# Performance work log

Hardware: AMD Instinct MI355X
Metric: run time of the kernel (lower is better)

## Reference

```python
import jax, jax.numpy as jnp
import numpy as np

S, N, LAT, HID, NH, NLAYERS = 8, 128, 128, 384, 8, 6
HT, WT, DT = 128, 128, 128
DIN, DOUT, RAD, LEVELS, FED = 1169, 3 + 3 * 128, 3, 4, 64


def sincos1d(d, pos):
    # MAE-style 1d sincos embedding, d even -> [..., d]
    omega = 1.0 / (10000.0 ** (jnp.arange(d // 2, dtype=jnp.float32) / (d / 2.0)))
    ang = pos[..., None] * omega
    return jnp.concatenate([jnp.sin(ang), jnp.cos(ang)], axis=-1)


def flow_embed(f, Cd=FED):
    # get_3d_embedding(flows, 64, cat_coords=True) -> [..., 3*Cd+3] = 195
    div = jnp.arange(0, Cd, 2, dtype=jnp.float32) * (1000.0 / Cd)
    outs = []
    for a in range(3):
        ang = f[..., a, None] * div
        pe = jnp.stack([jnp.sin(ang), jnp.cos(ang)], axis=-1).reshape(f.shape[:-1] + (Cd,))
        outs.append(pe)
    return jnp.concatenate(outs + [f], axis=-1)


def avg_pool2(x):
    B, Sv, Cc, H, W = x.shape
    return x.reshape(B, Sv, Cc, H // 2, 2, W // 2, 2).mean(axis=(4, 6))


def pyramid(fm):
    pyr = [fm]
    for _ in range(LEVELS - 1):
        fm = avg_pool2(fm)
        pyr.append(fm)
    return pyr


def bilinear_sample(corr, xy):
    # corr: [B,S,N,H,W]; xy: [B,S,N,P,2] pixel coords (x indexes W, y indexes H); zero padding
    B, Sv, Nn, H, W = corr.shape
    cf = corr.reshape(B, Sv, Nn, H * W)
    x, y = xy[..., 0], xy[..., 1]
    x0f = jnp.floor(x); y0f = jnp.floor(y)
    wx, wy = x - x0f, y - y0f
    x0 = x0f.astype(jnp.int32); y0 = y0f.astype(jnp.int32)

    def gather(xi, yi):
        ok = ((xi >= 0) & (xi < W) & (yi >= 0) & (yi < H)).astype(cf.dtype)
        idx = jnp.clip(yi, 0, H - 1) * W + jnp.clip(xi, 0, W - 1)
        v = jnp.take_along_axis(cf, idx.reshape(B, Sv, Nn, -1), axis=-1).reshape(idx.shape)
        return v * ok

    v00 = gather(x0, y0); v01 = gather(x0 + 1, y0)
    v10 = gather(x0, y0 + 1); v11 = gather(x0 + 1, y0 + 1)
    return v00 * (1 - wx) * (1 - wy) + v01 * wx * (1 - wy) + v10 * (1 - wx) * wy + v11 * wx * wy


def corr_sample(pyr, targets, coords):
    # RAFT/CoTracker CorrBlock: per-level dense correlation then (2r+1)^2 window bilinear lookup
    d = jnp.arange(-RAD, RAD + 1, dtype=jnp.float32)
    delta = jnp.stack(jnp.meshgrid(d, d, indexing="ij"), axis=-1).reshape(-1, 2)  # [49,2]
    scale = 1.0 / jnp.sqrt(jnp.float32(targets.shape[-1]))
    outs = []
    for l, fm in enumerate(pyr):
        corr = jnp.einsum("bsnc,bschw->bsnhw", targets, fm) * scale
        xy = coords[..., None, :] / (2.0 ** l) + delta
        outs.append(bilinear_sample(corr, xy))
    return jnp.concatenate(outs, axis=-1)  # [B,S,N,196]


def layernorm(x, g, b):
    m = x.mean(-1, keepdims=True)
    v = x.var(-1, keepdims=True)
    return (x - m) / jnp.sqrt(v + 1e-5) * g + b


def attention(x, Wqkv, bq, Wo, bo):
    M, T, H = x.shape
    dh = H // NH
    qkv = (x @ Wqkv + bq).reshape(M, T, 3, NH, dh)
    q, k, v = qkv[:, :, 0], qkv[:, :, 1], qkv[:, :, 2]
    att = jax.nn.softmax(jnp.einsum("mthd,mshd->mhts", q, k) / jnp.sqrt(jnp.float32(dh)), axis=-1)
    o = jnp.einsum("mhts,mshd->mthd", att, v).reshape(M, T, H)
    return o @ Wo + bo


def updateformer(x, support, W_in, b_in, lnp, Wqkv, bqkv, Wo, bo, W1, b1, W2, b2, W_out, b_out, Ws, bs):
    # x: [B,N,T,DIN]; alternating time (over T) and space (over N) pre-LN transformer blocks
    B, Np, T, _ = x.shape
    sproj = support @ Ws + bs  # [100,HID]
    h = x @ W_in + b_in + sproj.mean(axis=0)
    for i in range(NLAYERS):
        g1, bb1, g2, bb2 = lnp[i, 0], lnp[i, 1], lnp[i, 2], lnp[i, 3]
        if i % 2 == 0:
            y = h.reshape(B * Np, T, HID)
        else:
            y = h.transpose(0, 2, 1, 3).reshape(B * T, Np, HID)
        y = y + attention(layernorm(y, g1, bb1), Wqkv[i], bqkv[i], Wo[i], bo[i])
        z = layernorm(y, g2, bb2)
        y = y + jax.nn.gelu(z @ W1[i] + b1[i], approximate=False) @ W2[i] + b2[i]
        if i % 2 == 0:
            h = y.reshape(B, Np, T, HID)
        else:
            h = y.reshape(B, T, Np, HID).transpose(0, 2, 1, 3)
    return h @ W_out + b_out, sproj[None]


def groupnorm1(x, g, b):
    m = x.mean(-1, keepdims=True)
    v = x.var(-1, keepdims=True)
    return (x - m) / jnp.sqrt(v + 1e-5) * g + b


def _forward(fmapXY, fmapYZ, fmapXZ, coords_init, vis_init, track_mask, feat_init, support_features,
             W_in, b_in, lnp, Wqkv, bqkv, Wo, bo, W1, b1, W2, b2, W_out, b_out, Ws, bs,
             gn_g, gn_b, Wu, bu, Wvis, bvis, iters):
    B, Sv, Cc, H, W = fmapXY.shape
    D = fmapXZ.shape[-2]
    Nn = coords_init.shape[2]
    coords = coords_init
    ffeats = [feat_init[..., k] for k in range(3)]
    pyrXY, pyrYZ, pyrXZ = pyramid(fmapXY), pyramid(fmapYZ), pyramid(fmapXZ)
    grid_size = jnp.array([H, W, D], dtype=jnp.float32)
    # 3d sincos pos embed from query coords; 1169 padded to 1170 -> 390/axis, truncated back
    g = (coords[:, 0] / grid_size * 2.0 - 1.0) * 128.0  # [B,N,3]
    pe = jnp.concatenate([sincos1d(390, g[..., i]) for i in range(3)], axis=-1)[..., :DIN]
    pos_embed = pe.reshape(B * Nn, 1, DIN)
    times_embed = sincos1d(1170, jnp.arange(Sv, dtype=jnp.float32))[None, :, :DIN]
    support = support_features
    for _ in range(iters):
        coords = jax.lax.stop_gradient(coords)  # matches coords.detach()
        fxy = corr_sample(pyrXY, ffeats[0], coords[..., :2])
        fyz = corr_sample(pyrYZ, ffeats[1], coords[..., 1:3])
        fxz = corr_sample(pyrXZ, ffeats[2], coords[..., 0::2])
        fcorrs = jnp.concatenate([fxy, fyz, fxz], axis=-1)  # [B,S,N,588]
        fcorrs_ = fcorrs.transpose(0, 2, 1, 3).reshape(B * Nn, Sv, -1)
        flows_ = (coords - coords[:, :1]).transpose(0, 2, 1, 3).reshape(B * Nn, Sv, 3)
        flows_cat = flow_embed(flows_)  # [BN,S,195]
        ff = [f.transpose(0, 2, 1, 3).reshape(B * Nn, Sv, LAT) for f in ffeats]
        ffeats_ = jnp.concatenate(ff, axis=-1)  # [BN,S,384]
        # replicate torch's cat(dim=2)+permute+reshape layout exactly
        tmv = jnp.concatenate([track_mask, vis_init], axis=2).transpose(0, 2, 1, 3).reshape(B * Nn, Sv, 2)
        tin = jnp.concatenate([flows_cat, fcorrs_, ffeats_, tmv], axis=-1)  # [BN,S,1169]
        x = (tin + pos_embed + times_embed).reshape(B, Nn, Sv, DIN)
        delta, dse3 = updateformer(x, support, W_in, b_in, lnp, Wqkv, bqkv, Wo, bo, W1, b1, W2, b2, W_out, b_out, Ws, bs)
        support = support + dse3[0] / 100.0
        delta = delta.reshape(B * Nn, Sv, DOUT)
        d_coord = delta[..., :3].reshape(B, Nn, Sv, 3).transpose(0, 2, 1, 3)
        coords = coords + d_coord
        new_ffeats = []
        for k in range(3):
            dfk = delta[..., 3 + k * LAT:3 + (k + 1) * LAT]
            upd = jax.nn.gelu(groupnorm1(dfk, gn_g[k], gn_b[k]) @ Wu[k] + bu[k], approximate=False)
            new_ffeats.append(ffeats[k] + upd.reshape(B, Nn, Sv, LAT).transpose(0, 2, 1, 3))
        ffeats = new_ffeats
    vis = (jnp.concatenate(ffeats, axis=-1) @ Wvis + bvis)[..., 0]  # [B,S,N]
    return jnp.concatenate([coords, vis[..., None]], axis=-1)  # [B,S,N,4]


def setup_inputs() -> dict:
    key = jax.random.key(0)
    ks = jax.random.split(key, 16)
    f32 = jnp.float32
    B = 1
    fmapXY = jax.random.normal(ks[0], (B, S, LAT, HT, WT), f32)
    fmapYZ = jax.random.normal(ks[1], (B, S, LAT, DT, HT), f32)
    fmapXZ = jax.random.normal(ks[2], (B, S, LAT, DT, WT), f32)
    coords_init = jax.random.uniform(ks[3], (B, S, N, 3), f32) * 112.0 + 8.0
    vis_init = jnp.ones((B, S, N, 1), f32)
    track_mask = jnp.ones((B, S, N, 1), f32)
    feat_init = jax.random.normal(ks[4], (B, S, N, LAT, 3), f32)
    support_features = jnp.zeros((100, HID), f32) + 0.1
    w = lambda k, sh: jax.random.normal(k, sh, f32) * 0.02
    ln1 = jnp.stack([jnp.ones(HID, f32), jnp.zeros(HID, f32), jnp.ones(HID, f32), jnp.zeros(HID, f32)])
    params = dict(
        W_in=w(ks[5], (DIN, HID)), b_in=jnp.zeros((HID,), f32),
        lnp=jnp.tile(ln1[None], (NLAYERS, 1, 1)),
        Wqkv=w(ks[6], (NLAYERS, HID, 3 * HID)), bqkv=jnp.zeros((NLAYERS, 3 * HID), f32),
        Wo=w(ks[7], (NLAYERS, HID, HID)), bo=jnp.zeros((NLAYERS, HID), f32),
        W1=w(ks[8], (NLAYERS, HID, 4 * HID)), b1=jnp.zeros((NLAYERS, 4 * HID), f32),
        W2=w(ks[9], (NLAYERS, 4 * HID, HID)), b2=jnp.zeros((NLAYERS, HID), f32),
        W_out=w(ks[10], (HID, DOUT)), b_out=jnp.zeros((DOUT,), f32),
        Ws=w(ks[11], (HID, HID)), bs=jnp.zeros((HID,), f32),
        gn_g=jnp.ones((3, LAT), f32), gn_b=jnp.zeros((3, LAT), f32),
        Wu=w(ks[12], (3, LAT, LAT)), bu=jnp.zeros((3, LAT), f32),
        Wvis=w(ks[13], (3 * LAT, 1)), bvis=jnp.zeros((1,), f32),
    )
    return dict(fmapXY=fmapXY, fmapYZ=fmapYZ, fmapXZ=fmapXZ, coords_init=coords_init,
                vis_init=vis_init, track_mask=track_mask, feat_init=feat_init,
                support_features=support_features, iters=2, **params)


def reference(fmapXY, fmapYZ, fmapXZ, coords_init, vis_init, track_mask, feat_init, support_features,
              W_in, b_in, lnp, Wqkv, bqkv, Wo, bo, W1, b1, W2, b2, W_out, b_out, Ws, bs,
              gn_g, gn_b, Wu, bu, Wvis, bvis, iters):
    return _forward(fmapXY, fmapYZ, fmapXZ, coords_init, vis_init, track_mask, feat_init, support_features,
                    W_in, b_in, lnp, Wqkv, bqkv, Wo, bo, W1, b1, W2, b2, W_out, b_out, Ws, bs,
                    gn_g, gn_b, Wu, bu, Wvis, bvis, iters)
```

## Files before the change

kernel.cpp:

```cpp
#include <hip/hip_runtime.h>
#include <hip/hip_bf16.h>


#define DEVFN __device__ __forceinline__

typedef __attribute__((ext_vector_type(8))) short short8;
typedef __attribute__((ext_vector_type(4))) float f32x4;

static constexpr float INV_SQRT_DH = 0.14433756729740643f;
static constexpr float CORR_SCALE  = 0.08838834764831845f;
static constexpr size_t VSTRIDE = 22282240;

DEVFN float gelu_exact(float x){
  return 0.5f * x * (1.0f + erff(x * 0.7071067811865476f));
}
DEVFN short bf16_of(float f){
  __hip_bfloat16 b = __float2bfloat16(f);
  return *reinterpret_cast<short*>(&b);
}


__global__ void init_state_k(float* coords, const float* cinit,
                             float* ff, const float* feat_init,
                             float* support, const float* sfeat){
  int idx = blockIdx.x*256 + threadIdx.x;
  if (idx < 3072)  coords[idx]  = cinit[idx];
  if (idx < 49152){
    int row = idx / 384;
    support[idx] = (row < 100) ? sfeat[idx] : 0.0f;
  }
  if (idx < 393216){
    int k = idx / 131072, rest = idx % 131072;
    ff[idx] = feat_init[(size_t)rest*3 + k];
  }
}

__global__ void build_posE_k(float* posE, const float* cinit){
  int idx = blockIdx.x*256 + threadIdx.x;
  if (idx >= 128*1169) return;
  int n = idx / 1169, d = idx % 1169;
  int i = d / 390, dd = d % 390;
  float c = cinit[n*3 + i];
  float g = (c / 128.0f * 2.0f - 1.0f) * 128.0f;
  int m = (dd < 195) ? dd : dd - 195;
  float om = powf(10000.0f, -(float)m / 195.0f);
  float ang = g * om;
  posE[idx] = (dd < 195) ? sinf(ang) : cosf(ang);
}

__global__ void build_timE_k(float* timE){
  int idx = blockIdx.x*256 + threadIdx.x;
  if (idx >= 8*1169) return;
  int s = idx / 1169, d = idx % 1169;
  int m = (d < 585) ? d : d - 585;
  float om = powf(10000.0f, -(float)m / 585.0f);
  float ang = (float)s * om;
  timE[idx] = (d < 585) ? sinf(ang) : cosf(ang);
}

__global__ void transpose_cl_k(const float* __restrict__ in, __hip_bfloat16* __restrict__ out){
  __shared__ float tile[32][33];
  int s = blockIdx.z;
  int c0 = blockIdx.y*32, h0 = blockIdx.x*32;
  int tx = threadIdx.x & 31, ty = threadIdx.x >> 5;
  const float* ib = in + (size_t)s*128*16384;
  #pragma unroll
  for (int r=0;r<4;r++){
    int c = c0 + ty + r*8;
    tile[ty + r*8][tx] = ib[(size_t)c*16384 + h0 + tx];
  }
  __syncthreads();
  __hip_bfloat16* ob = out + (size_t)s*16384*128;
  #pragma unroll
  for (int r=0;r<4;r++){
    int hw = h0 + ty + r*8;
    ob[(size_t)hw*128 + c0 + tx] = __float2bfloat16(tile[tx][ty + r*8]);
  }
}

__global__ void pool2_k(const __hip_bfloat16* __restrict__ in, __hip_bfloat16* __restrict__ out, int So){
  int idx = blockIdx.x*256 + threadIdx.x;
  int total = 8*So*So*128;
  if (idx >= total) return;
  int c = idx & 127;
  int x = (idx >> 7) % So;
  int y = ((idx >> 7) / So) % So;
  int s = idx / (So*So*128);
  int Si = So*2;
  const __hip_bfloat16* b0 = in + (((size_t)s*Si + 2*y)*Si + 2*x)*128 + c;
  float v = __bfloat162float(b0[0]) + __bfloat162float(b0[128])
          + __bfloat162float(b0[(size_t)Si*128]) + __bfloat162float(b0[(size_t)Si*128 + 128]);
  out[idx] = __float2bfloat16(v*0.25f);
}

__global__ void wtrans_k(const float* __restrict__ in, __hip_bfloat16* __restrict__ out,
                         int K, int N, int Kpad, int Npad){
  __shared__ float tile[32][33];
  int z = blockIdx.z;
  const float* ib = in + (size_t)z*K*N;
  __hip_bfloat16* ob = out + (size_t)z*Npad*Kpad;
  int kb = blockIdx.y*32, nb = blockIdx.x*32;
  int tx = threadIdx.x & 31, ty = threadIdx.x >> 5;
  #pragma unroll
  for (int r=0;r<4;r++){
    int k = kb + ty + r*8, n = nb + tx;
    tile[ty+r*8][tx] = (k < K && n < N) ? ib[(size_t)k*N + n] : 0.0f;
  }
  __syncthreads();
  #pragma unroll
  for (int r=0;r<4;r++){
    int n = nb + ty + r*8, k = kb + tx;
    if (n < Npad && k < Kpad) ob[(size_t)n*Kpad + k] = __float2bfloat16(tile[tx][ty+r*8]);
  }
}

__global__ void corr_k(const __hip_bfloat16* __restrict__ pyr, const float* __restrict__ coords,
                       const float* __restrict__ ff, float* __restrict__ xbuf){
  __shared__ float t[128];
  __shared__ float p[64];
  int bid = blockIdx.x;
  int view = bid >> 10, s = (bid >> 7) & 7, n = bid & 127;
  int tid = threadIdx.x;
  t[tid]      = ff[(size_t)view*131072 + (size_t)(s*128+n)*128 + tid];
  t[tid + 64] = ff[(size_t)view*131072 + (size_t)(s*128+n)*128 + tid + 64];
  int ax = (view==1) ? 1 : 0;
  int ay = (view==0) ? 1 : 2;
  float X = coords[(s*128+n)*3 + ax];
  float Y = coords[(s*128+n)*3 + ay];
  const __hip_bfloat16* vb = pyr + (size_t)view*VSTRIDE;
  __syncthreads();
  size_t loff = 0;
  for (int l=0;l<4;l++){
    int sz = 128 >> l;
    float inv = 1.0f / (float)(1 << l);
    float cx = X * inv, cy = Y * inv;
    float x0f = floorf(cx), y0f = floorf(cy);
    float wx = cx - x0f, wy = cy - y0f;
    int ix0 = (int)x0f, iy0 = (int)y0f;
    int px = ix0 - 3 + (tid & 7);
    int py = iy0 - 3 + (tid >> 3);
    float acc = 0.0f;
    if (px >= 0 && px < sz && py >= 0 && py < sz){
      const uint2* row = reinterpret_cast<const uint2*>(vb + loff + (((size_t)s*sz + py)*sz + px)*128);
      #pragma unroll
      for (int c4=0;c4<32;c4++){
        uint2 u = row[c4];
        float f0 = __uint_as_float(u.x << 16);
        float f1 = __uint_as_float(u.x & 0xffff0000u);
        float f2 = __uint_as_float(u.y << 16);
        float f3 = __uint_as_float(u.y & 0xffff0000u);
        acc += t[c4*4+0]*f0 + t[c4*4+1]*f1 + t[c4*4+2]*f2 + t[c4*4+3]*f3;
      }
    }
    p[tid] = acc;
    __syncthreads();
    if (tid < 49){
      int i = tid / 7, jj = tid % 7;
      float v = p[jj*8+i]       * (1.0f-wx)*(1.0f-wy)
              + p[jj*8+i+1]     * wx*(1.0f-wy)
              + p[(jj+1)*8+i]   * (1.0f-wx)*wy
              + p[(jj+1)*8+i+1] * wx*wy;
      xbuf[(size_t)(n*8+s)*1184 + 195 + view*196 + l*49 + tid] = v * CORR_SCALE;
    }
    loff += (size_t)8*sz*sz*128;
    __syncthreads();
  }
}

__global__ void assemble_x_k(float* __restrict__ xbuf, const float* __restrict__ posE,
                             const float* __restrict__ timE, const float* __restrict__ coords,
                             const float* __restrict__ ff, const float* __restrict__ tmask,
                             const float* __restrict__ vinit){
  int r = blockIdx.x;
  int n = r >> 3, s = r & 7;
  for (int d = threadIdx.x; d < 1184; d += blockDim.x){
    float* dst = xbuf + (size_t)r*1184 + d;
    if (d >= 1169){ *dst = 0.0f; continue; }
    float base = posE[(size_t)n*1169 + d] + timE[(size_t)s*1169 + d];
    if (d >= 195 && d < 783){ *dst += base; continue; }
    float val;
    if (d < 195){
      if (d >= 192){
        int a = d - 192;
        val = coords[(s*128+n)*3 + a] - coords[n*3 + a];
      } else {
        int a = d >> 6, dd = d & 63;
        float f = coords[(s*128+n)*3 + a] - coords[n*3 + a];
        float ang = f * (31.25f * (float)(dd >> 1));
        val = (dd & 1) ? cosf(ang) : sinf(ang);
      }
    } else if (d < 1167){
      int cidx = d - 783, k = cidx >> 7, cc = cidx & 127;
      val = ff[(size_t)k*131072 + (size_t)(s*128+n)*128 + cc];
    } else {
      int c = d - 1167;
      int flat = n*16 + s*2 + c;
      int n2 = flat >> 3, s2 = flat & 7;
      val = (n2 < 128) ? tmask[s2*128 + n2] : vinit[s2*128 + (n2-128)];
    }
    *dst = val + base;
  }
}

__global__ void ln_rows_k(const float* __restrict__ in, int ld,
                          const float* __restrict__ g, const float* __restrict__ b,
                          __hip_bfloat16* __restrict__ out, int W){
  int wave = threadIdx.x >> 6, lane = threadIdx.x & 63;
  int r = blockIdx.x*4 + wave;
  const float* row = in + (size_t)r*ld;
  float x[6];
  float sum = 0.0f;
  #pragma unroll
  for (int e=0;e<6;e++) if (e*64 < W){ x[e] = row[lane + e*64]; sum += x[e]; }
  #pragma unroll
  for (int o=32;o>0;o>>=1) sum += __shfl_xor(sum, o);
  float mean = sum / (float)W;
  float vs = 0.0f;
  #pragma unroll
  for (int e=0;e<6;e++) if (e*64 < W){ float d = x[e]-mean; vs += d*d; }
  #pragma unroll
  for (int o=32;o>0;o>>=1) vs += __shfl_xor(vs, o);
  float invstd = 1.0f / sqrtf(vs/(float)W + 1e-5f);
  #pragma unroll
  for (int e=0;e<6;e++) if (e*64 < W){
    int cc = lane + e*64;
    out[(size_t)r*W + cc] = __float2bfloat16((x[e]-mean)*invstd*g[cc] + b[cc]);
  }
}

template<int K, int MODE, bool AF32>
__global__ __launch_bounds__(256) void mgemm_k(const void* __restrict__ A, int lda,
                                               const __hip_bfloat16* __restrict__ Bt,
                                               float* __restrict__ C, int ldc,
                                               int M, int N,
                                               const float* __restrict__ bias,
                                               float* __restrict__ aux,
                                               __hip_bfloat16* __restrict__ Cbf){
  constexpr int NSTEP = K/32;
  int tid = threadIdx.x;
  int lane = tid & 63, wid = tid >> 6;
  int wr = wid >> 1, wc = wid & 1;
  int lr = lane & 15, lk = lane >> 4;
  int m0 = blockIdx.y*64 + wr*32;
  int n0 = blockIdx.x*64 + wc*32;

  const __hip_bfloat16* Ab = (const __hip_bfloat16*)A;
  const float* Af = (const float*)A;
  size_t arow0 = (size_t)(m0 + lr)      * lda;
  size_t arow1 = (size_t)(m0 + 16 + lr) * lda;
  size_t brow0 = (size_t)(n0 + lr)      * K;
  size_t brow1 = (size_t)(n0 + 16 + lr) * K;

  f32x4 acc00 = {}, acc01 = {}, acc10 = {}, acc11 = {};

  auto loadAf = [&](size_t rowoff, int k0)->short8{
    if constexpr (AF32){
      const float* p = Af + rowoff + k0 + lk*8;
      short8 r;
      #pragma unroll
      for (int j=0;j<8;j++) r[j] = bf16_of(p[j]);
      return r;
    } else {
      return *reinterpret_cast<const short8*>(Ab + rowoff + k0 + lk*8);
    }
  };
  auto loadBf = [&](size_t rowoff, int k0)->short8{
    return *reinterpret_cast<const short8*>(Bt + rowoff + k0 + lk*8);
  };

  short8 a0 = loadAf(arow0,0), a1 = loadAf(arow1,0);
  short8 b0 = loadBf(brow0,0), b1 = loadBf(brow1,0);
  #pragma unroll
  for (int t=0;t<NSTEP;t++){
    short8 na0={}, na1={}, nb0={}, nb1={};
    if (t+1 < NSTEP){
      int k0 = (t+1)*32;
      na0 = loadAf(arow0,k0); na1 = loadAf(arow1,k0);
      nb0 = loadBf(brow0,k0); nb1 = loadBf(brow1,k0);
    }
    acc00 = __builtin_amdgcn_mfma_f32_16x16x32_bf16(a0,b0,acc00,0,0,0);
    acc01 = __builtin_amdgcn_mfma_f32_16x16x32_bf16(a0,b1,acc01,0,0,0);
    acc10 = __builtin_amdgcn_mfma_f32_16x16x32_bf16(a1,b0,acc10,0,0,0);
    acc11 = __builtin_amdgcn_mfma_f32_16x16x32_bf16(a1,b1,acc11,0,0,0);
    a0=na0; a1=na1; b0=nb0; b1=nb1;
  }

  f32x4 accs[2][2] = {{acc00, acc01},{acc10, acc11}};
  #pragma unroll
  for (int mi=0;mi<2;mi++){
    #pragma unroll
    for (int ni=0;ni<2;ni++){
      int c = n0 + ni*16 + lr;
      if (c >= N) continue;
      float bv = bias ? bias[c] : 0.0f;
      #pragma unroll
      for (int reg=0;reg<4;reg++){
        int r = m0 + mi*16 + lk*4 + reg;
        if (r >= M) continue;
        float v = accs[mi][ni][reg] + bv;
        if (MODE==0) C[(size_t)r*ldc + c] = v;
        else if (MODE==1) C[(size_t)r*ldc + c] += v;
        else if (MODE==2) Cbf[(size_t)r*ldc + c] = __float2bfloat16(gelu_exact(v));
        else {
          int ss = r & 7, nn2 = r >> 3;
          aux[((size_t)(ss*128+nn2))*128 + c] += gelu_exact(v);
        }
      }
    }
  }
}

__global__ void attn_even_k(const float* __restrict__ qkv, __hip_bfloat16* __restrict__ attout){
  int g = blockIdx.x;
  int tid = threadIdx.x;
  int h = tid >> 3, t = tid & 7;
  const float* qrow = qkv + (size_t)(g*8+t)*1152 + h*48;
  float q[48];
  #pragma unroll
  for (int d=0;d<48;d++) q[d] = qrow[d];
  float sc[8]; float mx = -1e30f;
  #pragma unroll
  for (int j=0;j<8;j++){
    const float* kr = qkv + (size_t)(g*8+j)*1152 + 384 + h*48;
    float sum = 0.0f;
    #pragma unroll
    for (int d=0;d<48;d++) sum += q[d]*kr[d];
    sum *= INV_SQRT_DH;
    sc[j] = sum; mx = fmaxf(mx, sum);
  }
  float l = 0.0f;
  #pragma unroll
  for (int j=0;j<8;j++){ sc[j] = expf(sc[j]-mx); l += sc[j]; }
  float o[48];
  #pragma unroll
  for (int d=0;d<48;d++) o[d] = 0.0f;
  #pragma unroll
  for (int j=0;j<8;j++){
    const float* vr = qkv + (size_t)(g*8+j)*1152 + 768 + h*48;
    float pj = sc[j];
    #pragma unroll
    for (int d=0;d<48;d++) o[d] += pj*vr[d];
  }
  float invl = 1.0f/l;
  __hip_bfloat16* orow = attout + (size_t)(g*8+t)*384 + h*48;
  #pragma unroll
  for (int d=0;d<48;d++) orow[d] = __float2bfloat16(o[d]*invl);
}

__global__ __launch_bounds__(256) void attn_odd_mfma_k(const float* __restrict__ qkv,
                                                       __hip_bfloat16* __restrict__ attout){
  __shared__ char smem[47872];
  __hip_bfloat16* Qb = (__hip_bfloat16*)smem;
  __hip_bfloat16* Kb = (__hip_bfloat16*)(smem + 18432);
  __hip_bfloat16* Pb = (__hip_bfloat16*)smem;
  __hip_bfloat16* Vt = (__hip_bfloat16*)(smem + 34816);
  int g = blockIdx.x & 7, h = blockIdx.x >> 3;
  int tid = threadIdx.x;

  for (int idx = tid; idx < 6144; idx += 256){
    int t = idx / 48, d = idx % 48;
    const float* row = qkv + (size_t)(t*8+g)*1152 + h*48;
    Qb[t*72+d] = __float2bfloat16(row[d]);
    Kb[t*72+d] = __float2bfloat16(row[384+d]);
  }
  for (int idx = tid; idx < 3072; idx += 256){
    int t = idx / 24, d = 48 + idx % 24;
    Qb[t*72+d] = __float2bfloat16(0.0f);
    Kb[t*72+d] = __float2bfloat16(0.0f);
  }
  __syncthreads();

  int lane = tid & 63, w = tid >> 6;
  int lr = lane & 15, lk = lane >> 4;
  int m0 = w*32;

  f32x4 S[2][8] = {};
  #pragma unroll
  for (int ks=0; ks<2; ks++){
    short8 a0 = *(const short8*)(Qb + (m0+lr)*72    + ks*32 + lk*8);
    short8 a1 = *(const short8*)(Qb + (m0+16+lr)*72 + ks*32 + lk*8);
    #pragma unroll
    for (int ni=0; ni<8; ni++){
      short8 b = *(const short8*)(Kb + (ni*16+lr)*72 + ks*32 + lk*8);
      S[0][ni] = __builtin_amdgcn_mfma_f32_16x16x32_bf16(a0,b,S[0][ni],0,0,0);
      S[1][ni] = __builtin_amdgcn_mfma_f32_16x16x32_bf16(a1,b,S[1][ni],0,0,0);
    }
  }

  #pragma unroll
  for (int mi=0;mi<2;mi++){
    #pragma unroll
    for (int reg=0;reg<4;reg++){
      float m = -1e30f;
      #pragma unroll
      for (int ni=0;ni<8;ni++) m = fmaxf(m, S[mi][ni][reg]);
      #pragma unroll
      for (int o=1;o<16;o<<=1) m = fmaxf(m, __shfl_xor(m, o));
      m *= INV_SQRT_DH;
      float l = 0.0f;
      #pragma unroll
      for (int ni=0;ni<8;ni++){
        float p = expf(S[mi][ni][reg]*INV_SQRT_DH - m);
        S[mi][ni][reg] = p;
        l += p;
      }
      #pragma unroll
      for (int o=1;o<16;o<<=1) l += __shfl_xor(l, o);
      float inv = 1.0f/l;
      #pragma unroll
      for (int ni=0;ni<8;ni++) S[mi][ni][reg] *= inv;
    }
  }
  __syncthreads();

  for (int idx = tid; idx < 6144; idx += 256){
    int j = idx / 48, d = idx % 48;
    Vt[d*136 + j] = __float2bfloat16(qkv[(size_t)(j*8+g)*1152 + 768 + h*48 + d]);
  }
  #pragma unroll
  for (int mi=0;mi<2;mi++)
    #pragma unroll
    for (int ni=0;ni<8;ni++)
      #pragma unroll
      for (int reg=0;reg<4;reg++)
        Pb[(m0+mi*16+lk*4+reg)*136 + ni*16+lr] = __float2bfloat16(S[mi][ni][reg]);
  __syncthreads();

  f32x4 O[2][3] = {};
  #pragma unroll
  for (int ks=0; ks<4; ks++){
    short8 a0 = *(const short8*)(Pb + (m0+lr)*136    + ks*32 + lk*8);
    short8 a1 = *(const short8*)(Pb + (m0+16+lr)*136 + ks*32 + lk*8);
    #pragma unroll
    for (int ni=0; ni<3; ni++){
      short8 b = *(const short8*)(Vt + (ni*16+lr)*136 + ks*32 + lk*8);
      O[0][ni] = __builtin_amdgcn_mfma_f32_16x16x32_bf16(a0,b,O[0][ni],0,0,0);
      O[1][ni] = __builtin_amdgcn_mfma_f32_16x16x32_bf16(a1,b,O[1][ni],0,0,0);
    }
  }
  #pragma unroll
  for (int mi=0;mi<2;mi++){
    #pragma unroll
    for (int ni=0;ni<3;ni++){
      #pragma unroll
      for (int reg=0;reg<4;reg++){
        int q = m0 + mi*16 + lk*4 + reg;
        int d = ni*16 + lr;
        attout[(size_t)(q*8+g)*384 + h*48 + d] = __float2bfloat16(O[mi][ni][reg]);
      }
    }
  }
}

__global__ void smean_k(const float* __restrict__ sproj, const float* __restrict__ b_in, float* __restrict__ bias2){
  int c = blockIdx.x*64 + threadIdx.x;
  if (c >= 384) return;
  float s = 0.0f;
  for (int r=0;r<100;r++) s += sproj[r*384 + c];
  bias2[c] = b_in[c] + s*0.01f;
}

__global__ void supp_upd_k(float* support, const float* sproj){
  int idx = blockIdx.x*256 + threadIdx.x;
  if (idx >= 38400) return;
  support[idx] += sproj[idx]*0.01f;
}

__global__ void coords_upd_k(float* coords, const float* dbuf){
  int idx = blockIdx.x*256 + threadIdx.x;
  if (idx >= 3072) return;
  int a = idx % 3, sn = idx / 3;
  int s = sn >> 7, n = sn & 127;
  coords[idx] += dbuf[(size_t)(n*8+s)*387 + a];
}

__global__ void final_out_k(const float* __restrict__ coords, const float* __restrict__ ff,
                            const float* __restrict__ Wvis, const float* __restrict__ bvis,
                            float* __restrict__ out){
  int sn = blockIdx.x*64 + threadIdx.x;
  if (sn >= 1024) return;
  float acc = bvis[0];
  for (int k=0;k<3;k++)
    for (int c=0;c<128;c++)
      acc += ff[(size_t)k*131072 + (size_t)sn*128 + c] * Wvis[k*128 + c];
  out[sn*4+0] = coords[sn*3+0];
  out[sn*4+1] = coords[sn*3+1];
  out[sn*4+2] = coords[sn*3+2];
  out[sn*4+3] = acc;
}


extern "C" void kernel_launch(void* const* d_in, const int* in_sizes, int n_in,
                              void* d_out, int out_size, void* d_ws, size_t ws_size,
                              hipStream_t stream) {
  const float* fmapXY   = (const float*)d_in[0];
  const float* fmapYZ   = (const float*)d_in[1];
  const float* fmapXZ   = (const float*)d_in[2];
  const float* cinit    = (const float*)d_in[3];
  const float* vinit    = (const float*)d_in[4];
  const float* tmask    = (const float*)d_in[5];
  const float* feat_init= (const float*)d_in[6];
  const float* sfeat    = (const float*)d_in[7];
  const float* W_in     = (const float*)d_in[9];
  const float* b_in     = (const float*)d_in[10];
  const float* lnp      = (const float*)d_in[11];
  const float* Wqkv     = (const float*)d_in[12];
  const float* bqkv     = (const float*)d_in[13];
  const float* Wo       = (const float*)d_in[14];
  const float* bo       = (const float*)d_in[15];
  const float* W1       = (const float*)d_in[16];
  const float* b1       = (const float*)d_in[17];
  const float* W2       = (const float*)d_in[18];
  const float* b2       = (const float*)d_in[19];
  const float* W_out    = (const float*)d_in[20];
  const float* b_out    = (const float*)d_in[21];
  const float* Ws       = (const float*)d_in[22];
  const float* bs       = (const float*)d_in[23];
  const float* gn_g     = (const float*)d_in[24];
  const float* gn_b     = (const float*)d_in[25];
  const float* Wu       = (const float*)d_in[26];
  const float* bu       = (const float*)d_in[27];
  const float* Wvis     = (const float*)d_in[28];
  const float* bvis     = (const float*)d_in[29];
  const int ITERS = 2;

  char* wp = (char*)d_ws;
  auto alloc = [&](size_t bytes)->char* {
    char* p = wp; wp += (bytes + 255) & ~(size_t)255; return p;
  };
  __hip_bfloat16* pyr = (__hip_bfloat16*)alloc(3ull*VSTRIDE*2);
  float* coords = (float*)alloc(3072ull*4);
  float* ff     = (float*)alloc(393216ull*4);
  float* support= (float*)alloc(49152ull*4);
  float* sproj  = (float*)alloc(38400ull*4);
  float* bias2  = (float*)alloc(384ull*4);
  float* posE   = (float*)alloc(149632ull*4);
  float* timE   = (float*)alloc(9352ull*4);
  float* xbuf   = (float*)alloc(1212416ull*4);
  float* h      = (float*)alloc(393216ull*4);
  float* qkvb   = (float*)alloc(1179648ull*4);
  float* dbuf   = (float*)alloc(396288ull*4);
  __hip_bfloat16* ybuf_bf = (__hip_bfloat16*)alloc(393216ull*2);
  __hip_bfloat16* atto_bf = (__hip_bfloat16*)alloc(393216ull*2);
  __hip_bfloat16* ffb_bf  = (__hip_bfloat16*)alloc(1572864ull*2);
  __hip_bfloat16* gtmp_bf = (__hip_bfloat16*)alloc(131072ull*2);
  __hip_bfloat16* WsT   = (__hip_bfloat16*)alloc(147456ull*2);
  __hip_bfloat16* WinT  = (__hip_bfloat16*)alloc(454656ull*2);
  __hip_bfloat16* WqkvT = (__hip_bfloat16*)alloc(2654208ull*2);
  __hip_bfloat16* WoT   = (__hip_bfloat16*)alloc(884736ull*2);
  __hip_bfloat16* W1T   = (__hip_bfloat16*)alloc(3538944ull*2);
  __hip_bfloat16* W2T   = (__hip_bfloat16*)alloc(3538944ull*2);
  __hip_bfloat16* WoutT = (__hip_bfloat16*)alloc(172032ull*2);
  __hip_bfloat16* WuT   = (__hip_bfloat16*)alloc(49152ull*2);
  if ((size_t)(wp - (char*)d_ws) > ws_size) return;

  init_state_k<<<1536, 256, 0, stream>>>(coords, cinit, ff, feat_init, support, sfeat);
  build_posE_k<<<(128*1169 + 255)/256, 256, 0, stream>>>(posE, cinit);
  build_timE_k<<<(8*1169 + 255)/256, 256, 0, stream>>>(timE);

  const float* fmaps[3] = {fmapXY, fmapYZ, fmapXZ};
  for (int v=0; v<3; v++){
    __hip_bfloat16* base = pyr + (size_t)v*VSTRIDE;
    transpose_cl_k<<<dim3(512,4,8), 256, 0, stream>>>(fmaps[v], base);
    pool2_k<<<(8*64*64*128 + 255)/256, 256, 0, stream>>>(base,              base + 16777216, 64);
    pool2_k<<<(8*32*32*128 + 255)/256, 256, 0, stream>>>(base + 16777216,   base + 20971520, 32);
    pool2_k<<<(8*16*16*128 + 255)/256, 256, 0, stream>>>(base + 20971520,   base + 22020096, 16);
  }

  wtrans_k<<<dim3(12,12,1), 256, 0, stream>>>(Ws,    WsT,   384, 384, 384, 384);
  wtrans_k<<<dim3(12,37,1), 256, 0, stream>>>(W_in,  WinT,  1169,384, 1184,384);
  wtrans_k<<<dim3(36,12,6), 256, 0, stream>>>(Wqkv,  WqkvT, 384, 1152,384, 1152);
  wtrans_k<<<dim3(12,12,6), 256, 0, stream>>>(Wo,    WoT,   384, 384, 384, 384);
  wtrans_k<<<dim3(48,12,6), 256, 0, stream>>>(W1,    W1T,   384, 1536,384, 1536);
  wtrans_k<<<dim3(12,48,6), 256, 0, stream>>>(W2,    W2T,   1536,384, 1536,384);
  wtrans_k<<<dim3(14,12,1), 256, 0, stream>>>(W_out, WoutT, 384, 387, 384, 448);
  wtrans_k<<<dim3(4,4,3),   256, 0, stream>>>(Wu,    WuT,   128, 128, 128, 128);

  for (int it=0; it<ITERS; ++it){
    corr_k<<<3072, 64, 0, stream>>>(pyr, coords, ff, xbuf);
    assemble_x_k<<<1024, 256, 0, stream>>>(xbuf, posE, timE, coords, ff, tmask, vinit);

    mgemm_k<384,0,true><<<dim3(6,2), 256, 0, stream>>>(support,384, WsT, sproj,384, 100,384, bs, nullptr, nullptr);
    smean_k<<<6, 64, 0, stream>>>(sproj, b_in, bias2);
    supp_upd_k<<<150, 256, 0, stream>>>(support, sproj);

    mgemm_k<1184,0,true><<<dim3(6,16), 256, 0, stream>>>(xbuf,1184, WinT, h,384, 1024,384, bias2, nullptr, nullptr);

    for (int i=0;i<6;i++){
      const float* g1  = lnp + (size_t)(i*4+0)*384;
      const float* bb1 = lnp + (size_t)(i*4+1)*384;
      const float* g2  = lnp + (size_t)(i*4+2)*384;
      const float* bb2 = lnp + (size_t)(i*4+3)*384;

      ln_rows_k<<<256, 256, 0, stream>>>(h, 384, g1, bb1, ybuf_bf, 384);
      mgemm_k<384,0,false><<<dim3(18,16), 256, 0, stream>>>(ybuf_bf,384, WqkvT + (size_t)i*442368,
                                                            qkvb,1152, 1024,1152, bqkv + i*1152, nullptr, nullptr);
      if ((i & 1) == 0) attn_even_k<<<128, 64, 0, stream>>>(qkvb, atto_bf);
      else              attn_odd_mfma_k<<<64, 256, 0, stream>>>(qkvb, atto_bf);
      mgemm_k<384,1,false><<<dim3(6,16), 256, 0, stream>>>(atto_bf,384, WoT + (size_t)i*147456,
                                                           h,384, 1024,384, bo + i*384, nullptr, nullptr);
      ln_rows_k<<<256, 256, 0, stream>>>(h, 384, g2, bb2, ybuf_bf, 384);
      mgemm_k<384,2,false><<<dim3(24,16), 256, 0, stream>>>(ybuf_bf,384, W1T + (size_t)i*589824,
                                                            nullptr,1536, 1024,1536, b1 + i*1536, nullptr, ffb_bf);
      mgemm_k<1536,1,false><<<dim3(6,16), 256, 0, stream>>>(ffb_bf,1536, W2T + (size_t)i*589824,
                                                            h,384, 1024,384, b2 + i*384, nullptr, nullptr);
    }

    mgemm_k<384,0,true><<<dim3(7,16), 256, 0, stream>>>(h,384, WoutT, dbuf,387, 1024,387, b_out, nullptr, nullptr);
    coords_upd_k<<<12, 256, 0, stream>>>(coords, dbuf);

    for (int k=0;k<3;k++){
      ln_rows_k<<<256, 256, 0, stream>>>(dbuf + 3 + k*128, 387, gn_g + k*128, gn_b + k*128, gtmp_bf, 128);
      mgemm_k<128,3,false><<<dim3(2,16), 256, 0, stream>>>(gtmp_bf,128, WuT + (size_t)k*16384,
                                                           nullptr,0, 1024,128, bu + k*128, ff + (size_t)k*131072, nullptr);
    }
  }

  final_out_k<<<16, 64, 0, stream>>>(coords, ff, Wvis, bvis, (float*)d_out);
}
```

Measured before the change: 1.595 ms.

## Fuse LayerNorm into QKV/FFN GEMMs, store QKV as bf16, batch GN/Wu launches

Adds a lngemm kernel that normalizes 64 rows of h into shared memory as bf16 and then runs the MFMA GEMM, replacing the separate ln_rows and GEMM launches for the QKV and FFN1 projections. The QKV output is now stored in bf16, which halves its traffic, and both attention kernels read it with vector loads. The three per-component group-norm plus Wu GEMM pairs become two batched launches, and the support mean and update kernels are merged into one. The trade-off is that every column block recomputes LayerNorm for its rows, which adds redundant work, and the bf16 rounding of QKV happens earlier in the even-layer attention path.

```diff
diff --git a/kernel.cpp b/kernel.cpp
--- a/kernel.cpp
+++ b/kernel.cpp
@@ -202,30 +202,29 @@
   }
 }
 
-__global__ void ln_rows_k(const float* __restrict__ in, int ld,
-                          const float* __restrict__ g, const float* __restrict__ b,
-                          __hip_bfloat16* __restrict__ out, int W){
+__global__ void gn_rows_k(const float* __restrict__ dbuf,
+                          const float* __restrict__ gn_g, const float* __restrict__ gn_b,
+                          __hip_bfloat16* __restrict__ gtmp){
+  int k = blockIdx.y;
+  const float* in = dbuf + 3 + k*128;
+  const float* g = gn_g + k*128;
+  const float* b = gn_b + k*128;
+  __hip_bfloat16* out = gtmp + (size_t)k*131072;
   int wave = threadIdx.x >> 6, lane = threadIdx.x & 63;
   int r = blockIdx.x*4 + wave;
-  const float* row = in + (size_t)r*ld;
-  float x[6];
-  float sum = 0.0f;
-  #pragma unroll
-  for (int e=0;e<6;e++) if (e*64 < W){ x[e] = row[lane + e*64]; sum += x[e]; }
+  const float* row = in + (size_t)r*387;
+  float x0 = row[lane], x1 = row[lane+64];
+  float sum = x0 + x1;
   #pragma unroll
   for (int o=32;o>0;o>>=1) sum += __shfl_xor(sum, o);
-  float mean = sum / (float)W;
-  float vs = 0.0f;
-  #pragma unroll
-  for (int e=0;e<6;e++) if (e*64 < W){ float d = x[e]-mean; vs += d*d; }
+  float mean = sum / 128.0f;
+  float d0 = x0-mean, d1 = x1-mean;
+  float vs = d0*d0 + d1*d1;
   #pragma unroll
   for (int o=32;o>0;o>>=1) vs += __shfl_xor(vs, o);
-  float invstd = 1.0f / sqrtf(vs/(float)W + 1e-5f);
-  #pragma unroll
-  for (int e=0;e<6;e++) if (e*64 < W){
-    int cc = lane + e*64;
-    out[(size_t)r*W + cc] = __float2bfloat16((x[e]-mean)*invstd*g[cc] + b[cc]);
-  }
+  float invstd = 1.0f / sqrtf(vs/128.0f + 1e-5f);
+  out[(size_t)r*128 + lane]      = __float2bfloat16(d0*invstd*g[lane] + b[lane]);
+  out[(size_t)r*128 + lane + 64] = __float2bfloat16(d1*invstd*g[lane+64] + b[lane+64]);
 }
 
 template<int K, int MODE, bool AF32>
@@ -234,8 +233,7 @@
                                                float* __restrict__ C, int ldc,
                                                int M, int N,
                                                const float* __restrict__ bias,
-                                               float* __restrict__ aux,
-                                               __hip_bfloat16* __restrict__ Cbf){
+                                               float* __restrict__ aux){
   constexpr int NSTEP = K/32;
   int tid = threadIdx.x;
   int lane = tid & 63, wid = tid >> 6;
@@ -300,7 +298,6 @@
         float v = accs[mi][ni][reg] + bv;
         if (MODE==0) C[(size_t)r*ldc + c] = v;
         else if (MODE==1) C[(size_t)r*ldc + c] += v;
-        else if (MODE==2) Cbf[(size_t)r*ldc + c] = __float2bfloat16(gelu_exact(v));
         else {
           int ss = r & 7, nn2 = r >> 3;
           aux[((size_t)(ss*128+nn2))*128 + c] += gelu_exact(v);
@@ -310,18 +307,148 @@
   }
 }
 
-__global__ void attn_even_k(const float* __restrict__ qkv, __hip_bfloat16* __restrict__ attout){
+template<bool GELU>
+__global__ __launch_bounds__(256) void lngemm_k(const float* __restrict__ A,
+                                                const float* __restrict__ gamma,
+                                                const float* __restrict__ beta,
+                                                const __hip_bfloat16* __restrict__ Bt,
+                                                __hip_bfloat16* __restrict__ Cbf, int ldc, int N,
+                                                const float* __restrict__ bias){
+  constexpr int LDSS = 392;
+  __shared__ short Asm[64*LDSS];
+  int tid = threadIdx.x, lane = tid & 63, w = tid >> 6;
+  int m0 = blockIdx.y*64, n0b = blockIdx.x*64;
+
+  float gg[6], bb[6];
+  #pragma unroll
+  for (int e=0;e<6;e++){ gg[e] = gamma[lane+e*64]; bb[e] = beta[lane+e*64]; }
+  for (int rr=0; rr<16; rr++){
+    int r = w*16 + rr;
+    const float* row = A + (size_t)(m0+r)*384;
+    float x[6]; float sum = 0.0f;
+    #pragma unroll
+    for (int e=0;e<6;e++){ x[e] = row[lane+e*64]; sum += x[e]; }
+    #pragma unroll
+    for (int o=32;o>0;o>>=1) sum += __shfl_xor(sum, o);
+    float mean = sum * (1.0f/384.0f);
+    float vs = 0.0f;
+    #pragma unroll
+    for (int e=0;e<6;e++){ float d = x[e]-mean; vs += d*d; }
+    #pragma unroll
+    for (int o=32;o>0;o>>=1) vs += __shfl_xor(vs, o);
+    float invstd = 1.0f / sqrtf(vs*(1.0f/384.0f) + 1e-5f);
+    #pragma unroll
+    for (int e=0;e<6;e++)
+      Asm[r*LDSS + lane + e*64] = bf16_of((x[e]-mean)*invstd*gg[e] + bb[e]);
+  }
+  __syncthreads();
+
+  int wr = w >> 1, wc = w & 1;
+  int lr = lane & 15, lk = lane >> 4;
+  const __hip_bfloat16* Brow0 = Bt + (size_t)(n0b + wc*32 + lr)*384;
+  const __hip_bfloat16* Brow1 = Brow0 + 16*384;
+  short8 b0 = *(const short8*)(Brow0 + lk*8);
+  short8 b1 = *(const short8*)(Brow1 + lk*8);
+  f32x4 acc00={}, acc01={}, acc10={}, acc11={};
+  #pragma unroll
+  for (int t=0;t<12;t++){
+    short8 a0 = *(const short8*)(&Asm[(wr*32+lr)*LDSS    + t*32 + lk*8]);
+    short8 a1 = *(const short8*)(&Asm[(wr*32+16+lr)*LDSS + t*32 + lk*8]);
+    short8 nb0={}, nb1={};
+    if (t < 11){
+      nb0 = *(const short8*)(Brow0 + (t+1)*32 + lk*8);
+      nb1 = *(const short8*)(Brow1 + (t+1)*32 + lk*8);
+    }
+    acc00 = __builtin_amdgcn_mfma_f32_16x16x32_bf16(a0,b0,acc00,0,0,0);
+    acc01 = __builtin_amdgcn_mfma_f32_16x16x32_bf16(a0,b1,acc01,0,0,0);
+    acc10 = __builtin_amdgcn_mfma_f32_16x16x32_bf16(a1,b0,acc10,0,0,0);
+    acc11 = __builtin_amdgcn_mfma_f32_16x16x32_bf16(a1,b1,acc11,0,0,0);
+    b0=nb0; b1=nb1;
+  }
+  f32x4 accs[2][2] = {{acc00, acc01},{acc10, acc11}};
+  #pragma unroll
+  for (int mi=0;mi<2;mi++){
+    #pragma unroll
+    for (int ni=0;ni<2;ni++){
+      int c = n0b + wc*32 + ni*16 + lr;
+      float bv = bias[c];
+      #pragma unroll
+      for (int reg=0;reg<4;reg++){
+        int r = m0 + wr*32 + mi*16 + lk*4 + reg;
+        float v = accs[mi][ni][reg] + bv;
+        Cbf[(size_t)r*ldc + c] = __float2bfloat16(GELU ? gelu_exact(v) : v);
+      }
+    }
+  }
+}
+
+__global__ __launch_bounds__(256) void wu_gemm_k(const __hip_bfloat16* __restrict__ gtmp,
+                                                 const __hip_bfloat16* __restrict__ WuT,
+                                                 const float* __restrict__ bu,
+                                                 float* __restrict__ ff){
+  int z = blockIdx.z;
+  const __hip_bfloat16* A  = gtmp + (size_t)z*131072;
+  const __hip_bfloat16* Bt = WuT  + (size_t)z*16384;
+  const float* bias = bu + (size_t)z*128;
+  float* aux = ff + (size_t)z*131072;
+  int tid = threadIdx.x, lane = tid & 63, wid = tid >> 6;
+  int wr = wid >> 1, wc = wid & 1;
+  int lr = lane & 15, lk = lane >> 4;
+  int m0 = blockIdx.y*64 + wr*32;
+  int n0 = blockIdx.x*64 + wc*32;
+  const short8* A0 = (const short8*)(A + (size_t)(m0+lr)*128);
+  const short8* A1 = (const short8*)(A + (size_t)(m0+16+lr)*128);
+  const short8* B0 = (const short8*)(Bt + (size_t)(n0+lr)*128);
+  const short8* B1 = (const short8*)(Bt + (size_t)(n0+16+lr)*128);
+  f32x4 acc00={}, acc01={}, acc10={}, acc11={};
+  #pragma unroll
+  for (int t=0;t<4;t++){
+    short8 a0 = A0[t*4 + lk], a1 = A1[t*4 + lk];
+    short8 b0 = B0[t*4 + lk], b1 = B1[t*4 + lk];
+    acc00 = __builtin_amdgcn_mfma_f32_16x16x32_bf16(a0,b0,acc00,0,0,0);
+    acc01 = __builtin_amdgcn_mfma_f32_16x16x32_bf16(a0,b1,acc01,0,0,0);
+    acc10 = __builtin_amdgcn_mfma_f32_16x16x32_bf16(a1,b0,acc10,0,0,0);
+    acc11 = __builtin_amdgcn_mfma_f32_16x16x32_bf16(a1,b1,acc11,0,0,0);
+  }
+  f32x4 accs[2][2] = {{acc00, acc01},{acc10, acc11}};
+  #pragma unroll
+  for (int mi=0;mi<2;mi++){
+    #pragma unroll
+    for (int ni=0;ni<2;ni++){
+      int c = n0 + ni*16 + lr;
+      float bv = bias[c];
+      #pragma unroll
+      for (int reg=0;reg<4;reg++){
+        int r = m0 + mi*16 + lk*4 + reg;
+        float v = accs[mi][ni][reg] + bv;
+        int ss = r & 7, nn2 = r >> 3;
+        aux[((size_t)(ss*128+nn2))*128 + c] += gelu_exact(v);
+      }
+    }
+  }
+}
+
+DEVFN void load48bf(const __hip_bfloat16* p, float* q){
+  const uint32_t* u = (const uint32_t*)p;
+  #pragma unroll
+  for (int i=0;i<24;i++){
+    uint32_t w = u[i];
+    q[2*i]   = __uint_as_float(w << 16);
+    q[2*i+1] = __uint_as_float(w & 0xffff0000u);
+  }
+}
+
+__global__ void attn_even_k(const __hip_bfloat16* __restrict__ qkv, __hip_bfloat16* __restrict__ attout){
   int g = blockIdx.x;
   int tid = threadIdx.x;
   int h = tid >> 3, t = tid & 7;
-  const float* qrow = qkv + (size_t)(g*8+t)*1152 + h*48;
   float q[48];
-  #pragma unroll
-  for (int d=0;d<48;d++) q[d] = qrow[d];
+  load48bf(qkv + (size_t)(g*8+t)*1152 + h*48, q);
   float sc[8]; float mx = -1e30f;
   #pragma unroll
   for (int j=0;j<8;j++){
-    const float* kr = qkv + (size_t)(g*8+j)*1152 + 384 + h*48;
+    float kr[48];
+    load48bf(qkv + (size_t)(g*8+j)*1152 + 384 + h*48, kr);
     float sum = 0.0f;
     #pragma unroll
     for (int d=0;d<48;d++) sum += q[d]*kr[d];
@@ -336,7 +463,8 @@
   for (int d=0;d<48;d++) o[d] = 0.0f;
   #pragma unroll
   for (int j=0;j<8;j++){
-    const float* vr = qkv + (size_t)(g*8+j)*1152 + 768 + h*48;
+    float vr[48];
+    load48bf(qkv + (size_t)(g*8+j)*1152 + 768 + h*48, vr);
     float pj = sc[j];
     #pragma unroll
     for (int d=0;d<48;d++) o[d] += pj*vr[d];
@@ -347,26 +475,28 @@
   for (int d=0;d<48;d++) orow[d] = __float2bfloat16(o[d]*invl);
 }
 
-__global__ __launch_bounds__(256) void attn_odd_mfma_k(const float* __restrict__ qkv,
+__global__ __launch_bounds__(256) void attn_odd_mfma_k(const __hip_bfloat16* __restrict__ qkv,
                                                        __hip_bfloat16* __restrict__ attout){
   __shared__ char smem[47872];
-  __hip_bfloat16* Qb = (__hip_bfloat16*)smem;
-  __hip_bfloat16* Kb = (__hip_bfloat16*)(smem + 18432);
-  __hip_bfloat16* Pb = (__hip_bfloat16*)smem;
-  __hip_bfloat16* Vt = (__hip_bfloat16*)(smem + 34816);
+  short* Qb = (short*)smem;
+  short* Kb = (short*)(smem + 18432);
+  short* Pb = (short*)smem;
+  short* Vt = (short*)(smem + 34816);
   int g = blockIdx.x & 7, h = blockIdx.x >> 3;
   int tid = threadIdx.x;
 
-  for (int idx = tid; idx < 6144; idx += 256){
-    int t = idx / 48, d = idx % 48;
-    const float* row = qkv + (size_t)(t*8+g)*1152 + h*48;
-    Qb[t*72+d] = __float2bfloat16(row[d]);
-    Kb[t*72+d] = __float2bfloat16(row[384+d]);
-  }
-  for (int idx = tid; idx < 3072; idx += 256){
-    int t = idx / 24, d = 48 + idx % 24;
-    Qb[t*72+d] = __float2bfloat16(0.0f);
-    Kb[t*72+d] = __float2bfloat16(0.0f);
+  const short* qs = (const short*)qkv;
+  for (int idx = tid; idx < 768; idx += 256){
+    int t = idx / 6, dblk = idx % 6;
+    size_t base = (size_t)(t*8+g)*1152 + h*48 + dblk*8;
+    *(short8*)(Qb + t*72 + dblk*8) = *(const short8*)(qs + base);
+    *(short8*)(Kb + t*72 + dblk*8) = *(const short8*)(qs + base + 384);
+  }
+  short8 zz = {};
+  for (int idx = tid; idx < 384; idx += 256){
+    int t = idx / 3, dblk = idx % 3;
+    *(short8*)(Qb + t*72 + 48 + dblk*8) = zz;
+    *(short8*)(Kb + t*72 + 48 + dblk*8) = zz;
   }
   __syncthreads();
 
@@ -413,9 +543,11 @@
   }
   __syncthreads();
 
-  for (int idx = tid; idx < 6144; idx += 256){
-    int j = idx / 48, d = idx % 48;
-    Vt[d*136 + j] = __float2bfloat16(qkv[(size_t)(j*8+g)*1152 + 768 + h*48 + d]);
+  for (int idx = tid; idx < 768; idx += 256){
+    int j = idx / 6, dblk = idx % 6;
+    short8 v = *(const short8*)(qs + (size_t)(j*8+g)*1152 + 768 + h*48 + dblk*8);
+    #pragma unroll
+    for (int e=0;e<8;e++) Vt[(dblk*8+e)*136 + j] = v[e];
   }
   #pragma unroll
   for (int mi=0;mi<2;mi++)
@@ -423,7 +555,7 @@
     for (int ni=0;ni<8;ni++)
       #pragma unroll
       for (int reg=0;reg<4;reg++)
-        Pb[(m0+mi*16+lk*4+reg)*136 + ni*16+lr] = __float2bfloat16(S[mi][ni][reg]);
+        Pb[(m0+mi*16+lk*4+reg)*136 + ni*16+lr] = bf16_of(S[mi][ni][reg]);
   __syncthreads();
 
   f32x4 O[2][3] = {};
@@ -452,18 +584,16 @@
   }
 }
 
-__global__ void smean_k(const float* __restrict__ sproj, const float* __restrict__ b_in, float* __restrict__ bias2){
-  int c = blockIdx.x*64 + threadIdx.x;
-  if (c >= 384) return;
-  float s = 0.0f;
-  for (int r=0;r<100;r++) s += sproj[r*384 + c];
-  bias2[c] = b_in[c] + s*0.01f;
-}
-
-__global__ void supp_upd_k(float* support, const float* sproj){
+__global__ void supp_smean_k(const float* __restrict__ sproj, const float* __restrict__ b_in,
+                             float* __restrict__ bias2, float* __restrict__ support){
   int idx = blockIdx.x*256 + threadIdx.x;
-  if (idx >= 38400) return;
-  support[idx] += sproj[idx]*0.01f;
+  if (idx < 38400) support[idx] += sproj[idx]*0.01f;
+  else if (idx < 38784){
+    int c = idx - 38400;
+    float s = 0.0f;
+    for (int r=0;r<100;r++) s += sproj[r*384 + c];
+    bias2[c] = b_in[c] + s*0.01f;
+  }
 }
 
 __global__ void coords_upd_k(float* coords, const float* dbuf){
@@ -538,12 +668,11 @@
   float* timE   = (float*)alloc(9352ull*4);
   float* xbuf   = (float*)alloc(1212416ull*4);
   float* h      = (float*)alloc(393216ull*4);
-  float* qkvb   = (float*)alloc(1179648ull*4);
   float* dbuf   = (float*)alloc(396288ull*4);
-  __hip_bfloat16* ybuf_bf = (__hip_bfloat16*)alloc(393216ull*2);
+  __hip_bfloat16* qkv_bf  = (__hip_bfloat16*)alloc(1179648ull*2);
   __hip_bfloat16* atto_bf = (__hip_bfloat16*)alloc(393216ull*2);
   __hip_bfloat16* ffb_bf  = (__hip_bfloat16*)alloc(1572864ull*2);
-  __hip_bfloat16* gtmp_bf = (__hip_bfloat16*)alloc(131072ull*2);
+  __hip_bfloat16* gtmp_bf = (__hip_bfloat16*)alloc(393216ull*2);
   __hip_bfloat16* WsT   = (__hip_bfloat16*)alloc(147456ull*2);
   __hip_bfloat16* WinT  = (__hip_bfloat16*)alloc(454656ull*2);
   __hip_bfloat16* WqkvT = (__hip_bfloat16*)alloc(2654208ull*2);
@@ -580,11 +709,10 @@
     corr_k<<<3072, 64, 0, stream>>>(pyr, coords, ff, xbuf);
     assemble_x_k<<<1024, 256, 0, stream>>>(xbuf, posE, timE, coords, ff, tmask, vinit);
 
-    mgemm_k<384,0,true><<<dim3(6,2), 256, 0, stream>>>(support,384, WsT, sproj,384, 100,384, bs, nullptr, nullptr);
-    smean_k<<<6, 64, 0, stream>>>(sproj, b_in, bias2);
-    supp_upd_k<<<150, 256, 0, stream>>>(support, sproj);
-
-    mgemm_k<1184,0,true><<<dim3(6,16), 256, 0, stream>>>(xbuf,1184, WinT, h,384, 1024,384, bias2, nullptr, nullptr);
+    mgemm_k<384,0,true><<<dim3(6,2), 256, 0, stream>>>(support,384, WsT, sproj,384, 100,384, bs, nullptr);
+    supp_smean_k<<<152, 256, 0, stream>>>(sproj, b_in, bias2, support);
+
+    mgemm_k<1184,0,true><<<dim3(6,16), 256, 0, stream>>>(xbuf,1184, WinT, h,384, 1024,384, bias2, nullptr);
 
     for (int i=0;i<6;i++){
       const float* g1  = lnp + (size_t)(i*4+0)*384;
@@ -592,28 +720,23 @@
       const float* g2  = lnp + (size_t)(i*4+2)*384;
       const float* bb2 = lnp + (size_t)(i*4+3)*384;
 
-      ln_rows_k<<<256, 256, 0, stream>>>(h, 384, g1, bb1, ybuf_bf, 384);
-      mgemm_k<384,0,false><<<dim3(18,16), 256, 0, stream>>>(ybuf_bf,384, WqkvT + (size_t)i*442368,
-                                                            qkvb,1152, 1024,1152, bqkv + i*1152, nullptr, nullptr);
-      if ((i & 1) == 0) attn_even_k<<<128, 64, 0, stream>>>(qkvb, atto_bf);
-      else              attn_odd_mfma_k<<<64, 256, 0, stream>>>(qkvb, atto_bf);
+      lngemm_k<false><<<dim3(18,16), 256, 0, stream>>>(h, g1, bb1, WqkvT + (size_t)i*442368,
+                                                       qkv_bf, 1152, 1152, bqkv + i*1152);
+      if ((i & 1) == 0) attn_even_k<<<128, 64, 0, stream>>>(qkv_bf, atto_bf);
+      else              attn_odd_mfma_k<<<64, 256, 0, stream>>>(qkv_bf, atto_bf);
       mgemm_k<384,1,false><<<dim3(6,16), 256, 0, stream>>>(atto_bf,384, WoT + (size_t)i*147456,
-                                                           h,384, 1024,384, bo + i*384, nullptr, nullptr);
-      ln_rows_k<<<256, 256, 0, stream>>>(h, 384, g2, bb2, ybuf_bf, 384);
-      mgemm_k<384,2,false><<<dim3(24,16), 256, 0, stream>>>(ybuf_bf,384, W1T + (size_t)i*589824,
-                                                            nullptr,1536, 1024,1536, b1 + i*1536, nullptr, ffb_bf);
+                                                           h,384, 1024,384, bo + i*384, nullptr);
+      lngemm_k<true><<<dim3(24,16), 256, 0, stream>>>(h, g2, bb2, W1T + (size_t)i*589824,
+                                                      ffb_bf, 1536, 1536, b1 + i*1536);
       mgemm_k<1536,1,false><<<dim3(6,16), 256, 0, stream>>>(ffb_bf,1536, W2T + (size_t)i*589824,
-                                                            h,384, 1024,384, b2 + i*384, nullptr, nullptr);
-    }
-
-    mgemm_k<384,0,true><<<dim3(7,16), 256, 0, stream>>>(h,384, WoutT, dbuf,387, 1024,387, b_out, nullptr, nullptr);
+                                                            h,384, 1024,384, b2 + i*384, nullptr);
+    }
+
+    mgemm_k<384,0,true><<<dim3(7,16), 256, 0, stream>>>(h,384, WoutT, dbuf,387, 1024,387, b_out, nullptr);
     coords_upd_k<<<12, 256, 0, stream>>>(coords, dbuf);
 
-    for (int k=0;k<3;k++){
-      ln_rows_k<<<256, 256, 0, stream>>>(dbuf + 3 + k*128, 387, gn_g + k*128, gn_b + k*128, gtmp_bf, 128);
-      mgemm_k<128,3,false><<<dim3(2,16), 256, 0, stream>>>(gtmp_bf,128, WuT + (size_t)k*16384,
-                                                           nullptr,0, 1024,128, bu + k*128, ff + (size_t)k*131072, nullptr);
-    }
+    gn_rows_k<<<dim3(256,3), 256, 0, stream>>>(dbuf, gn_g, gn_b, gtmp_bf);
+    wu_gemm_k<<<dim3(2,16,3), 256, 0, stream>>>(gtmp_bf, WuT, bu, ff);
   }
 
   final_out_k<<<16, 64, 0, stream>>>(coords, ff, Wvis, bvis, (float*)d_out);
```

Result: faster. 1.545 ms (-3.1%).
